# Kernel optimization log

Measured on AMD Instinct MI355X. Metric: run time of the kernel, lower is better.

The kernel has to match this reference:

```python
import jax, jax.numpy as jnp
import numpy as np

B = 8192          # batch
NUM_PROTOS = 10   # num_prototypes
NUM_CLASSES = 10
N_PATCHES = 14 * 14  # 196 non-overlapping 2x2 patches of a 28x28 image


def setup_inputs() -> dict:
    key = jax.random.key(0)
    k1, k2, k3 = jax.random.split(key, 3)
    x = jax.random.normal(k1, (B, 784), dtype=jnp.float32)
    prototypes = jax.random.normal(k2, (NUM_PROTOS, 4), dtype=jnp.float32)
    W = jax.random.normal(k3, (NUM_CLASSES, NUM_PROTOS * N_PATCHES), dtype=jnp.float32) * 0.02
    b = jnp.zeros((NUM_CLASSES,), dtype=jnp.float32)
    return {"x": x, "prototypes": prototypes, "W": W, "b": b}


def _features(x, prototypes):
    # x: (B, 784) -> non-overlapping 2x2 patches, row-major within each patch
    bsz = x.shape[0]
    img = x.reshape(bsz, 28, 28)
    patches = img.reshape(bsz, 14, 2, 14, 2).transpose(0, 1, 3, 2, 4).reshape(bsz, N_PATCHES, 4)
    # Quantum kernel: ansatz applies RY(x_i) then RY(-y_i) per wire on |0000>.
    # |0...0> amplitude factorizes over the 4 wires: prod_i cos((x_i - y_i)/2).
    diff = patches[:, :, None, :] - prototypes[None, None, :, :]   # (B, 196, P, 4)
    kern = jnp.abs(jnp.prod(jnp.cos(0.5 * diff), axis=-1))          # (B, 196, P)
    # torch stacks per-prototype then permutes to (B, P, 196) and flattens
    return kern.transpose(0, 2, 1).reshape(bsz, -1)                 # (B, P*196)


def reference(x, prototypes, W, b):
    feats = _features(x, prototypes)
    logits = feats @ W.T + b
    return jax.nn.log_softmax(logits, axis=-1)
```

## Files before the change

kernel.cpp:

```cpp
#include <hip/hip_runtime.h>
#include <math.h>

#define B_ROWS 8192
#define NPROTO 10
#define NCLS 10
#define NPATCH 196

#define TABLE_OFF 0
#define WT2_OFF   80
#define WT2_ELEMS (NPATCH * NPROTO * NCLS)
#define WS_NEEDED ((size_t)(WT2_OFF + WT2_ELEMS) * sizeof(float))

__global__ __launch_bounds__(256) void quanv_prep(
    const float* __restrict__ W, const float* __restrict__ protos,
    float* __restrict__ ws, float* __restrict__ out, int buildWt2) {
  int idx = blockIdx.x * 256 + threadIdx.x;
  if (idx < NPROTO * 8) {
    int proto = idx >> 3;
    int j = idx & 7;
    float h = 0.5f * protos[proto * 4 + (j & 3)];
    ws[TABLE_OFF + idx] = (j < 4) ? __cosf(h) : __sinf(h);
  }
  if (buildWt2 && idx < WT2_ELEMS) {
    int p     = idx / (NPROTO * NCLS);
    int rem   = idx - p * (NPROTO * NCLS);
    int proto = rem / NCLS;
    int c     = rem - proto * NCLS;
    ws[WT2_OFF + idx] = W[c * (NPROTO * NPATCH) + proto * NPATCH + p];
  }
  if (idx < B_ROWS * NCLS) out[idx] = 0.0f;
}

template <bool USE_WT2>
__global__ __launch_bounds__(256) void quanv_main(
    const float* __restrict__ x, const float* __restrict__ ws,
    const float* __restrict__ W, float* __restrict__ out) {
  __shared__ float red[64 * NCLS];

  const int tid = threadIdx.x;
  for (int i = tid; i < 64 * NCLS; i += 256) red[i] = 0.0f;
  __syncthreads();

  const int wid  = __builtin_amdgcn_readfirstlane(tid >> 6);
  const int lane = tid & 63;
  const int r    = blockIdx.x * 64 + lane;
  const int pr   = blockIdx.y;

  const float* tb  = ws + TABLE_OFF;
  const float* Wt2 = ws + WT2_OFF;

  const int pj0 = (wid < 2) ? wid * 4 : 8 + (wid - 2) * 3;
  const int npj = (wid < 2) ? 4 : 3;

  float acc[NCLS];
#pragma unroll
  for (int c = 0; c < NCLS; ++c) acc[c] = 0.0f;

  const float* xr = x + (size_t)r * 784 + pr * 56;

  for (int j = 0; j < npj; ++j) {
    int pj = pj0 + j;
    int p  = pr * 14 + pj;
    float2 a01 = *(const float2*)(xr + 2 * pj);
    float2 a23 = *(const float2*)(xr + 2 * pj + 28);
    float s0, c0, s1, c1, s2, c2, s3, c3;
    __sincosf(0.5f * a01.x, &s0, &c0);
    __sincosf(0.5f * a01.y, &s1, &c1);
    __sincosf(0.5f * a23.x, &s2, &c2);
    __sincosf(0.5f * a23.y, &s3, &c3);

#pragma unroll
    for (int proto = 0; proto < NPROTO; ++proto) {
      const float* t8 = tb + proto * 8;
      float t0 = fmaf(c0, t8[0], s0 * t8[4]);
      float t1 = fmaf(c1, t8[1], s1 * t8[5]);
      float t2 = fmaf(c2, t8[2], s2 * t8[6]);
      float t3 = fmaf(c3, t8[3], s3 * t8[7]);
      float q  = fabsf((t0 * t1) * (t2 * t3));
#pragma unroll
      for (int c = 0; c < NCLS; ++c) {
        float w = USE_WT2 ? Wt2[p * (NPROTO * NCLS) + proto * NCLS + c]
                          : W[c * (NPROTO * NPATCH) + proto * NPATCH + p];
        acc[c] = fmaf(q, w, acc[c]);
      }
    }
  }

#pragma unroll
  for (int c = 0; c < NCLS; ++c) atomicAdd(&red[lane * NCLS + c], acc[c]);
  __syncthreads();

  for (int i = tid; i < 64 * NCLS; i += 256) {
    atomicAdd(&out[(size_t)blockIdx.x * 64 * NCLS + i], red[i]);
  }
}

__global__ __launch_bounds__(256) void quanv_softmax(
    float* __restrict__ out, const float* __restrict__ bias) {
  int r = blockIdx.x * 256 + threadIdx.x;
  float v[NCLS];
  float m = -1e30f;
#pragma unroll
  for (int c = 0; c < NCLS; ++c) {
    v[c] = out[r * NCLS + c] + bias[c];
    m = fmaxf(m, v[c]);
  }
  float sum = 0.0f;
#pragma unroll
  for (int c = 0; c < NCLS; ++c) sum += __expf(v[c] - m);
  float lse = m + __logf(sum);
#pragma unroll
  for (int c = 0; c < NCLS; ++c) out[r * NCLS + c] = v[c] - lse;
}

extern "C" void kernel_launch(void* const* d_in, const int* in_sizes, int n_in,
                              void* d_out, int out_size, void* d_ws, size_t ws_size,
                              hipStream_t stream) {
  const float* x      = (const float*)d_in[0];
  const float* protos = (const float*)d_in[1];
  const float* W      = (const float*)d_in[2];
  const float* bias   = (const float*)d_in[3];
  float* out = (float*)d_out;
  float* ws  = (float*)d_ws;

  const bool useWt2 = (ws_size >= WS_NEEDED);

  quanv_prep<<<(B_ROWS * NCLS + 255) / 256, 256, 0, stream>>>(W, protos, ws, out, useWt2 ? 1 : 0);

  dim3 grid(B_ROWS / 64, 14);
  if (useWt2)
    quanv_main<true><<<grid, 256, 0, stream>>>(x, ws, W, out);
  else
    quanv_main<false><<<grid, 256, 0, stream>>>(x, ws, W, out);

  quanv_softmax<<<B_ROWS / 256, 256, 0, stream>>>(out, bias);
}
```

Before: 108.8 us.

## Stage x tile in LDS, widen blocks to two patch rows, replace atomics with partials

New measurement: 91.34 us. 16.1% less time.

```diff
diff --git a/kernel.cpp b/kernel.cpp
--- a/kernel.cpp
+++ b/kernel.cpp
@@ -3,17 +3,17 @@
 
 #define B_ROWS 8192
 #define NPROTO 10
-#define NCLS 10
+#define NCLS   10
 #define NPATCH 196
 
 #define TABLE_OFF 0
-#define WT2_OFF   80
-#define WT2_ELEMS (NPATCH * NPROTO * NCLS)
-#define WS_NEEDED ((size_t)(WT2_OFF + WT2_ELEMS) * sizeof(float))
+#define WT2_OFF   128
+#define PART_OFF  19776
+#define XS_STRIDE 113
 
 __global__ __launch_bounds__(256) void quanv_prep(
     const float* __restrict__ W, const float* __restrict__ protos,
-    float* __restrict__ ws, float* __restrict__ out, int buildWt2) {
+    float* __restrict__ ws) {
   int idx = blockIdx.x * 256 + threadIdx.x;
   if (idx < NPROTO * 8) {
     int proto = idx >> 3;
@@ -21,54 +21,61 @@
     float h = 0.5f * protos[proto * 4 + (j & 3)];
     ws[TABLE_OFF + idx] = (j < 4) ? __cosf(h) : __sinf(h);
   }
-  if (buildWt2 && idx < WT2_ELEMS) {
+  if (idx < NPATCH * NPROTO * NCLS) {
     int p     = idx / (NPROTO * NCLS);
     int rem   = idx - p * (NPROTO * NCLS);
     int proto = rem / NCLS;
     int c     = rem - proto * NCLS;
     ws[WT2_OFF + idx] = W[c * (NPROTO * NPATCH) + proto * NPATCH + p];
   }
-  if (idx < B_ROWS * NCLS) out[idx] = 0.0f;
 }
 
-template <bool USE_WT2>
 __global__ __launch_bounds__(256) void quanv_main(
     const float* __restrict__ x, const float* __restrict__ ws,
-    const float* __restrict__ W, float* __restrict__ out) {
-  __shared__ float red[64 * NCLS];
+    float* __restrict__ partial) {
+  __shared__ float xs[64 * XS_STRIDE];
+  __shared__ float red[4 * 64 * 11];
 
   const int tid = threadIdx.x;
-  for (int i = tid; i < 64 * NCLS; i += 256) red[i] = 0.0f;
+  const int bx  = blockIdx.x;
+  const int pr2 = blockIdx.y;
+
+  {
+    const float* src = x + (size_t)bx * 64 * 784 + pr2 * 112;
+    for (int i = tid; i < 64 * 28; i += 256) {
+      int row = i / 28, quad = i - row * 28;
+      float4 v = *(const float4*)(src + (size_t)row * 784 + quad * 4);
+      float* d = &xs[row * XS_STRIDE + quad * 4];
+      d[0] = v.x; d[1] = v.y; d[2] = v.z; d[3] = v.w;
+    }
+  }
   __syncthreads();
 
   const int wid  = __builtin_amdgcn_readfirstlane(tid >> 6);
   const int lane = tid & 63;
-  const int r    = blockIdx.x * 64 + lane;
-  const int pr   = blockIdx.y;
-
   const float* tb  = ws + TABLE_OFF;
   const float* Wt2 = ws + WT2_OFF;
-
-  const int pj0 = (wid < 2) ? wid * 4 : 8 + (wid - 2) * 3;
-  const int npj = (wid < 2) ? 4 : 3;
+  const float* xr  = &xs[lane * XS_STRIDE];
 
   float acc[NCLS];
 #pragma unroll
   for (int c = 0; c < NCLS; ++c) acc[c] = 0.0f;
 
-  const float* xr = x + (size_t)r * 784 + pr * 56;
+  for (int j = 0; j < 7; ++j) {
+    int lp  = wid * 7 + j;
+    int piL = lp >= 14 ? 1 : 0;
+    int pj  = lp - piL * 14;
+    int off = piL * 56 + 2 * pj;
+    float x0 = xr[off],      x1 = xr[off + 1];
+    float x2 = xr[off + 28], x3 = xr[off + 29];
+    float s0, c0, s1, c1, s2, c2, s3, c3;
+    __sincosf(0.5f * x0, &s0, &c0);
+    __sincosf(0.5f * x1, &s1, &c1);
+    __sincosf(0.5f * x2, &s2, &c2);
+    __sincosf(0.5f * x3, &s3, &c3);
 
-  for (int j = 0; j < npj; ++j) {
-    int pj = pj0 + j;
-    int p  = pr * 14 + pj;
-    float2 a01 = *(const float2*)(xr + 2 * pj);
-    float2 a23 = *(const float2*)(xr + 2 * pj + 28);
-    float s0, c0, s1, c1, s2, c2, s3, c3;
-    __sincosf(0.5f * a01.x, &s0, &c0);
-    __sincosf(0.5f * a01.y, &s1, &c1);
-    __sincosf(0.5f * a23.x, &s2, &c2);
-    __sincosf(0.5f * a23.y, &s3, &c3);
-
+    int p = pr2 * 28 + lp;
+    const float* wp = Wt2 + p * (NPROTO * NCLS);
 #pragma unroll
     for (int proto = 0; proto < NPROTO; ++proto) {
       const float* t8 = tb + proto * 8;
@@ -77,34 +84,45 @@
       float t2 = fmaf(c2, t8[2], s2 * t8[6]);
       float t3 = fmaf(c3, t8[3], s3 * t8[7]);
       float q  = fabsf((t0 * t1) * (t2 * t3));
+      const float* wq = wp + proto * NCLS;
 #pragma unroll
-      for (int c = 0; c < NCLS; ++c) {
-        float w = USE_WT2 ? Wt2[p * (NPROTO * NCLS) + proto * NCLS + c]
-                          : W[c * (NPROTO * NPATCH) + proto * NPATCH + p];
-        acc[c] = fmaf(q, w, acc[c]);
-      }
+      for (int c = 0; c < NCLS; ++c) acc[c] = fmaf(q, wq[c], acc[c]);
     }
   }
 
+  {
+    float* myred = &red[(tid >> 6) * (64 * 11) + lane * 11];
 #pragma unroll
-  for (int c = 0; c < NCLS; ++c) atomicAdd(&red[lane * NCLS + c], acc[c]);
+    for (int c = 0; c < NCLS; ++c) myred[c] = acc[c];
+  }
   __syncthreads();
 
   for (int i = tid; i < 64 * NCLS; i += 256) {
-    atomicAdd(&out[(size_t)blockIdx.x * 64 * NCLS + i], red[i]);
+    int row = i / NCLS, c = i - row * NCLS;
+    int o = row * 11 + c;
+    float s = red[o] + red[704 + o] + red[1408 + o] + red[2112 + o];
+    partial[((size_t)pr2 * B_ROWS + (size_t)bx * 64 + row) * NCLS + c] = s;
   }
 }
 
-__global__ __launch_bounds__(256) void quanv_softmax(
-    float* __restrict__ out, const float* __restrict__ bias) {
+__global__ __launch_bounds__(256) void quanv_final(
+    const float* __restrict__ partial, const float* __restrict__ bias,
+    float* __restrict__ out) {
   int r = blockIdx.x * 256 + threadIdx.x;
   float v[NCLS];
-  float m = -1e30f;
 #pragma unroll
-  for (int c = 0; c < NCLS; ++c) {
-    v[c] = out[r * NCLS + c] + bias[c];
-    m = fmaxf(m, v[c]);
+  for (int c = 0; c < NCLS; ++c) v[c] = bias[c];
+  for (int y = 0; y < 7; ++y) {
+    const float* pp = partial + ((size_t)y * B_ROWS + r) * NCLS;
+#pragma unroll
+    for (int c = 0; c < NCLS; c += 2) {
+      float2 t = *(const float2*)(pp + c);
+      v[c] += t.x; v[c + 1] += t.y;
+    }
   }
+  float m = v[0];
+#pragma unroll
+  for (int c = 1; c < NCLS; ++c) m = fmaxf(m, v[c]);
   float sum = 0.0f;
 #pragma unroll
   for (int c = 0; c < NCLS; ++c) sum += __expf(v[c] - m);
@@ -123,15 +141,7 @@
   float* out = (float*)d_out;
   float* ws  = (float*)d_ws;
 
-  const bool useWt2 = (ws_size >= WS_NEEDED);
-
-  quanv_prep<<<(B_ROWS * NCLS + 255) / 256, 256, 0, stream>>>(W, protos, ws, out, useWt2 ? 1 : 0);
-
-  dim3 grid(B_ROWS / 64, 14);
-  if (useWt2)
-    quanv_main<true><<<grid, 256, 0, stream>>>(x, ws, W, out);
-  else
-    quanv_main<false><<<grid, 256, 0, stream>>>(x, ws, W, out);
-
-  quanv_softmax<<<B_ROWS / 256, 256, 0, stream>>>(out, bias);
+  quanv_prep<<<(NPATCH * NPROTO * NCLS + 255) / 256, 256, 0, stream>>>(W, protos, ws);
+  quanv_main<<<dim3(B_ROWS / 64, 7), 256, 0, stream>>>(x, ws, ws + PART_OFF);
+  quanv_final<<<B_ROWS / 256, 256, 0, stream>>>(ws + PART_OFF, bias, out);
 }
```
